# Optimization experiments

Hardware: AMD Instinct MI355X
Metric: run time of the kernel (lower is better)

Reference implementation:

```python
import jax, jax.numpy as jnp
import numpy as np

N_DST0 = 20000  # number of dst nodes of block0 == src nodes of block1


def _graph_conv(x, src, dst, n_dst, W, b):
    # DGL GraphConv with norm='both': D_in^{-1/2} A D_out^{-1/2} X W + b
    e_ones = jnp.ones(src.shape[0], dtype=x.dtype)
    deg_out = jax.ops.segment_sum(e_ones, src, num_segments=x.shape[0])
    deg_in = jax.ops.segment_sum(e_ones, dst, num_segments=n_dst)
    xs = x * jax.lax.rsqrt(jnp.maximum(deg_out, 1.0))[:, None]
    agg = jax.ops.segment_sum(xs[src], dst, num_segments=n_dst)  # [n_dst, F]
    agg = agg * jax.lax.rsqrt(jnp.maximum(deg_in, 1.0))[:, None]
    return agg @ W + b


def setup_inputs() -> dict:
    key = jax.random.key(0)
    ks = jax.random.split(key, 10)
    vocab, emb, hid, out = 50000, 128, 256, 16
    n_src0, n_dst0, n_dst1 = 50000, N_DST0, 5000
    e0, e1 = 300000, 75000
    return {
        "user_word": jax.random.randint(ks[0], (n_src0, 10, 5), 0, vocab),
        "labels": jax.random.randint(ks[1], (n_dst1,), 0, out),
        "src0": jax.random.randint(ks[2], (e0,), 0, n_src0),
        "dst0": jax.random.randint(ks[3], (e0,), 0, n_dst0),
        "src1": jax.random.randint(ks[4], (e1,), 0, n_dst0),
        "dst1": jax.random.randint(ks[5], (e1,), 0, n_dst1),
        "word_table": jax.random.normal(ks[6], (vocab, emb), jnp.float32),
        "W1": jax.random.normal(ks[7], (emb, hid), jnp.float32) * 0.05,
        "b1": jnp.zeros((hid,), jnp.float32),
        "W2": jax.random.normal(ks[8], (hid, out), jnp.float32) * 0.05,
        "b2": jnp.zeros((out,), jnp.float32),
    }


def reference(user_word, labels, src0, dst0, src1, dst1, word_table, W1, b1, W2, b2):
    n_dst1 = labels.shape[0]
    # embedding gather + mean over words (dim=2) then items (dim=1)
    wf = word_table[user_word]                    # [n_src0, n_items, n_words, emb]
    x = jnp.mean(jnp.mean(wf, axis=2), axis=1)    # [n_src0, emb]
    x = jax.nn.relu(_graph_conv(x, src0, dst0, N_DST0, W1, b1))
    x = jax.nn.relu(_graph_conv(x, src1, dst1, n_dst1, W2, b2))
    x = x[:n_dst1]
    return (x, labels)
```

## Files before the change

### kernel.cpp

```cpp
#include <hip/hip_runtime.h>

#define E0     300000
#define E1     75000
#define NSRC0  50000
#define NDST0  20000
#define NDST1  5000
#define EMB    128
#define HID    256
#define NOUT   16

#define NPB        40
#define TILE_SHIFT 12
#define NEMB_BLK   (NSRC0 / NPB)

#define X0S  32.0f
#define H1S  64.0f

typedef __attribute__((ext_vector_type(8))) short bf16x8;
typedef __attribute__((ext_vector_type(4))) float f32x4;
typedef __attribute__((ext_vector_type(2))) float f32x2;

__device__ __forceinline__ unsigned short f2bf(float f) {
    unsigned u = __float_as_uint(f);
    return (unsigned short)((u + 0x7FFFu + ((u >> 16) & 1u)) >> 16);
}
__device__ __forceinline__ unsigned pack2(float a, float b) {
    return (unsigned)f2bf(a) | ((unsigned)f2bf(b) << 16);
}
__device__ __forceinline__ unsigned pack4_fp8(float a0, float a1, float a2, float a3) {
    unsigned p = 0;
    p = __builtin_amdgcn_cvt_pk_fp8_f32(a0, a1, p, false);
    p = __builtin_amdgcn_cvt_pk_fp8_f32(a2, a3, p, true);
    return p;
}
__device__ __forceinline__ unsigned char f2fp8(float v) {
    unsigned p = __builtin_amdgcn_cvt_pk_fp8_f32(v, v, 0, false);
    return (unsigned char)(p & 0xFF);
}
#if __has_builtin(__builtin_amdgcn_cvt_pk_f32_fp8)
__device__ __forceinline__ f32x2 up_lo(unsigned v) { return __builtin_amdgcn_cvt_pk_f32_fp8(v, false); }
__device__ __forceinline__ f32x2 up_hi(unsigned v) { return __builtin_amdgcn_cvt_pk_f32_fp8(v, true); }
#else
__device__ __forceinline__ f32x2 up_lo(unsigned v) {
    f32x2 r; r.x = __builtin_amdgcn_cvt_f32_fp8(v, 0); r.y = __builtin_amdgcn_cvt_f32_fp8(v, 1); return r;
}
__device__ __forceinline__ f32x2 up_hi(unsigned v) {
    f32x2 r; r.x = __builtin_amdgcn_cvt_f32_fp8(v, 2); r.y = __builtin_amdgcn_cvt_f32_fp8(v, 3); return r;
}
#endif

__global__ void prep_kernel(const float* __restrict__ wt, unsigned char* __restrict__ wt8,
                            const float* __restrict__ W1, unsigned short* __restrict__ W1Tb,
                            const float* __restrict__ W2, unsigned short* __restrict__ W2Tb,
                            const int* __restrict__ src0, const int* __restrict__ dst0,
                            const int* __restrict__ src1, const int* __restrict__ dst1,
                            int* cnt0, int* cnt1, int* degO0, int* degO1) {
    int i = blockIdx.x * blockDim.x + threadIdx.x;
    if (i < NSRC0 * EMB / 8) {
        const float4* in = (const float4*)wt;
        float4 v0 = in[i * 2], v1 = in[i * 2 + 1];
        uint2 o;
        o.x = pack4_fp8(v0.x, v0.y, v0.z, v0.w);
        o.y = pack4_fp8(v1.x, v1.y, v1.z, v1.w);
        ((uint2*)wt8)[i] = o;
    }
    if (i < EMB * HID) {
        int n = i & 255, k = i >> 8;
        W1Tb[n * 128 + k] = f2bf(W1[i]);
    }
    if (i < HID * NOUT) {
        int n = i & 15, k = i >> 4;
        W2Tb[n * 256 + k] = f2bf(W2[i]);
    }
    if (i < E0) {
        atomicAdd(&cnt0[dst0[i]], 1);
        atomicAdd(&degO0[src0[i]], 1);
    }
    if (i < E1) {
        atomicAdd(&cnt1[dst1[i]], 1);
        atomicAdd(&degO1[src1[i]], 1);
    }
}

__device__ void scan_body(const int* __restrict__ cnt, int n,
                          int* __restrict__ off, int* __restrict__ cur) {
    __shared__ int sums[1024];
    int t = threadIdx.x;
    int chunk = (n + 1023) / 1024;
    int lo = t * chunk, hi = min(lo + chunk, n);
    int s = 0;
    for (int i = lo; i < hi; ++i) s += cnt[i];
    sums[t] = s;
    __syncthreads();
    for (int d = 1; d < 1024; d <<= 1) {
        int x = (t >= d) ? sums[t - d] : 0;
        __syncthreads();
        sums[t] += x;
        __syncthreads();
    }
    int run = (t == 0) ? 0 : sums[t - 1];
    for (int i = lo; i < hi; ++i) {
        off[i] = run; cur[i] = run;
        run += cnt[i];
    }
    if (t == 1023) off[n] = run;
}

__global__ void scan_kernel(const int* cnt0, int* off0, int* cur0,
                            const int* cnt1, int* off1, int* cur1) {
    if (blockIdx.x == 0) scan_body(cnt0, NDST0, off0, cur0);
    else                 scan_body(cnt1, NDST1, off1, cur1);
}

__global__ void embed_bucket_kernel(const int* __restrict__ user_word,
                                    const unsigned char* __restrict__ wt8,
                                    const int* __restrict__ degO0,
                                    unsigned char* __restrict__ x0f,
                                    const int* __restrict__ src0, const int* __restrict__ dst0,
                                    const int* __restrict__ src1, const int* __restrict__ dst1,
                                    int* cur0, int* cur1, int* esrc0, int* esrc1) {
    if (blockIdx.x & 1) {
        int i = (blockIdx.x >> 1) * 256 + threadIdx.x;
        if (i < E0) {
            int p = atomicAdd(&cur0[dst0[i]], 1);
            esrc0[p] = src0[i];
        }
        if (i < E1) {
            int p = atomicAdd(&cur1[dst1[i]], 1);
            esrc1[p] = src1[i];
        }
        return;
    }
    int eb = blockIdx.x >> 1;
    __shared__ int raw[NPB * 50];
    __shared__ int srt[NPB * 50];
    __shared__ int cnt[NPB * 17];
    int t = threadIdx.x;
    int base = eb * NPB * 50;
    for (int j = t; j < NPB * 50; j += 256)
        raw[j] = user_word[base + j];
    for (int j = t; j < NPB * 17; j += 256)
        cnt[j] = 0;
    __syncthreads();
    if (t < NPB) {
        int* c = cnt + t * 17;
        const int* r = raw + t * 50;
        for (int j = 0; j < 50; ++j) c[r[j] >> TILE_SHIFT]++;
        int run = 0;
        for (int b = 0; b < 13; ++b) { int v = c[b]; c[b] = run; run += v; }
        int* o = srt + t * 50;
        for (int j = 0; j < 50; ++j) { int v = r[j]; o[c[v >> TILE_SHIFT]++] = v; }
    }
    __syncthreads();
    int g = t >> 5, l = t & 31;
    const unsigned* wt4 = (const unsigned*)wt8;
    const int* id0 = srt + (g     ) * 50;
    const int* id1 = srt + (g +  8) * 50;
    const int* id2 = srt + (g + 16) * 50;
    const int* id3 = srt + (g + 24) * 50;
    const int* id4 = srt + (g + 32) * 50;
    f32x2 a01[5], a23[5];
    #pragma unroll
    for (int k = 0; k < 5; ++k) { a01[k] = (f32x2){0.f, 0.f}; a23[k] = (f32x2){0.f, 0.f}; }
    for (int j = 0; j < 50; j += 2) {
        unsigned v0a = wt4[id0[j] * 32 + l], v0b = wt4[id0[j + 1] * 32 + l];
        unsigned v1a = wt4[id1[j] * 32 + l], v1b = wt4[id1[j + 1] * 32 + l];
        unsigned v2a = wt4[id2[j] * 32 + l], v2b = wt4[id2[j + 1] * 32 + l];
        unsigned v3a = wt4[id3[j] * 32 + l], v3b = wt4[id3[j + 1] * 32 + l];
        unsigned v4a = wt4[id4[j] * 32 + l], v4b = wt4[id4[j + 1] * 32 + l];
        a01[0] += up_lo(v0a) + up_lo(v0b); a23[0] += up_hi(v0a) + up_hi(v0b);
        a01[1] += up_lo(v1a) + up_lo(v1b); a23[1] += up_hi(v1a) + up_hi(v1b);
        a01[2] += up_lo(v2a) + up_lo(v2b); a23[2] += up_hi(v2a) + up_hi(v2b);
        a01[3] += up_lo(v3a) + up_lo(v3b); a23[3] += up_hi(v3a) + up_hi(v3b);
        a01[4] += up_lo(v4a) + up_lo(v4b); a23[4] += up_hi(v4a) + up_hi(v4b);
    }
    #pragma unroll
    for (int k = 0; k < 5; ++k) {
        int node = eb * NPB + g + k * 8;
        float s = rsqrtf(fmaxf((float)degO0[node], 1.0f)) * (0.02f * X0S);
        ((unsigned*)x0f)[node * 32 + l] =
            pack4_fp8(a01[k].x * s, a01[k].y * s, a23[k].x * s, a23[k].y * s);
    }
}

__global__ void agg1_kernel(const int* __restrict__ off0, const int* __restrict__ esrc0,
                            const unsigned char* __restrict__ x0f,
                            unsigned short* __restrict__ agg1b) {
    int d = blockIdx.x;
    int t = threadIdx.x;
    int half = t >> 5, l = t & 31;
    int lo = off0[d], hi = off0[d + 1];
    const unsigned* x4 = (const unsigned*)x0f;
    f32x2 a01a = {0.f, 0.f}, a23a = {0.f, 0.f};
    f32x2 a01b = {0.f, 0.f}, a23b = {0.f, 0.f};
    int j = lo + half;
    for (; j + 2 < hi; j += 4) {
        unsigned va = x4[esrc0[j] * 32 + l];
        unsigned vb = x4[esrc0[j + 2] * 32 + l];
        a01a += up_lo(va); a23a += up_hi(va);
        a01b += up_lo(vb); a23b += up_hi(vb);
    }
    if (j < hi) {
        unsigned v = x4[esrc0[j] * 32 + l];
        a01a += up_lo(v); a23a += up_hi(v);
    }
    f32x2 a01 = a01a + a01b, a23 = a23a + a23b;
    a01.x += __shfl_down(a01.x, 32); a01.y += __shfl_down(a01.y, 32);
    a23.x += __shfl_down(a23.x, 32); a23.y += __shfl_down(a23.y, 32);
    if (half == 0) {
        float sc = rsqrtf(fmaxf((float)(hi - lo), 1.0f)) * (1.0f / X0S);
        uint2 o; o.x = pack2(a01.x * sc, a01.y * sc); o.y = pack2(a23.x * sc, a23.y * sc);
        ((uint2*)agg1b)[d * 32 + l] = o;
    }
}

__global__ void gemm1_kernel(const unsigned short* __restrict__ agg1b,
                             const int* __restrict__ degO1,
                             const unsigned short* __restrict__ W1Tb,
                             const float* __restrict__ b1,
                             unsigned char* __restrict__ h1f) {
    __shared__ float s_out[16];
    int t = threadIdx.x;
    int row0 = blockIdx.x * 16;
    if (t < 16) s_out[t] = rsqrtf(fmaxf((float)degO1[row0 + t], 1.0f)) * H1S;
    __syncthreads();
    int w = t >> 6, lane = t & 63;
    int m = lane & 15, quad = lane >> 4;
    const unsigned short* abase = agg1b + (row0 + m) * 128 + quad * 8;
    bf16x8 afr[4];
    #pragma unroll
    for (int ks = 0; ks < 4; ++ks)
        afr[ks] = *(const bf16x8*)(abase + ks * 32);
    #pragma unroll
    for (int ct = 0; ct < 4; ++ct) {
        int gcol0 = (w * 4 + ct) * 16;
        const unsigned short* bbase = W1Tb + (gcol0 + m) * 128 + quad * 8;
        f32x4 acc = {0.f, 0.f, 0.f, 0.f};
        #pragma unroll
        for (int ks = 0; ks < 4; ++ks) {
            bf16x8 bfr = *(const bf16x8*)(bbase + ks * 32);
            acc = __builtin_amdgcn_mfma_f32_16x16x32_bf16(afr[ks], bfr, acc, 0, 0, 0);
        }
        int gcol = gcol0 + m;
        float bb = b1[gcol];
        #pragma unroll
        for (int reg = 0; reg < 4; ++reg) {
            int row = quad * 4 + reg;
            h1f[(row0 + row) * 256 + gcol] = f2fp8(fmaxf(acc[reg] + bb, 0.f) * s_out[row]);
        }
    }
}

__global__ void agg2_kernel(const int* __restrict__ off1, const int* __restrict__ esrc1,
                            const unsigned char* __restrict__ h1f,
                            unsigned short* __restrict__ agg2b) {
    int d = blockIdx.x;
    int l = threadIdx.x;
    int lo = off1[d], hi = off1[d + 1];
    const unsigned* h4 = (const unsigned*)h1f;
    f32x2 a01 = {0.f, 0.f}, a23 = {0.f, 0.f};
    int j = lo;
    for (; j + 3 < hi; j += 4) {
        unsigned v0 = h4[esrc1[j] * 64 + l];
        unsigned v1 = h4[esrc1[j + 1] * 64 + l];
        unsigned v2 = h4[esrc1[j + 2] * 64 + l];
        unsigned v3 = h4[esrc1[j + 3] * 64 + l];
        a01 += up_lo(v0) + up_lo(v1) + up_lo(v2) + up_lo(v3);
        a23 += up_hi(v0) + up_hi(v1) + up_hi(v2) + up_hi(v3);
    }
    for (; j < hi; ++j) {
        unsigned v = h4[esrc1[j] * 64 + l];
        a01 += up_lo(v); a23 += up_hi(v);
    }
    float sc = rsqrtf(fmaxf((float)(hi - lo), 1.0f)) * (1.0f / H1S);
    uint2 o; o.x = pack2(a01.x * sc, a01.y * sc); o.y = pack2(a23.x * sc, a23.y * sc);
    ((uint2*)agg2b)[d * 64 + l] = o;
}

__global__ void gemm2_kernel(const unsigned short* __restrict__ agg2b,
                             const unsigned short* __restrict__ W2Tb,
                             const float* __restrict__ b2,
                             const int* __restrict__ labels,
                             float* __restrict__ out) {
    int lane = threadIdx.x;
    int row0 = blockIdx.x * 16;
    int m = lane & 15, quad = lane >> 4;
    int arow = min(row0 + m, NDST1 - 1);
    const unsigned short* abase = agg2b + arow * 256 + quad * 8;
    const unsigned short* bbase = W2Tb + m * 256 + quad * 8;
    f32x4 acc = {0.f, 0.f, 0.f, 0.f};
    #pragma unroll
    for (int ks = 0; ks < 8; ++ks) {
        bf16x8 af = *(const bf16x8*)(abase + ks * 32);
        bf16x8 bf = *(const bf16x8*)(bbase + ks * 32);
        acc = __builtin_amdgcn_mfma_f32_16x16x32_bf16(af, bf, acc, 0, 0, 0);
    }
    float bb = b2[m];
    #pragma unroll
    for (int reg = 0; reg < 4; ++reg) {
        int row = row0 + quad * 4 + reg;
        if (row < NDST1)
            out[row * NOUT + m] = fmaxf(acc[reg] + bb, 0.f);
    }
    if (lane < 16 && row0 + lane < NDST1)
        out[NDST1 * NOUT + row0 + lane] = (float)labels[row0 + lane];
}

extern "C" void kernel_launch(void* const* d_in, const int* in_sizes, int n_in,
                              void* d_out, int out_size, void* d_ws, size_t ws_size,
                              hipStream_t stream) {
    const int*   user_word  = (const int*)d_in[0];
    const int*   labels     = (const int*)d_in[1];
    const int*   src0       = (const int*)d_in[2];
    const int*   dst0       = (const int*)d_in[3];
    const int*   src1       = (const int*)d_in[4];
    const int*   dst1       = (const int*)d_in[5];
    const float* word_table = (const float*)d_in[6];
    const float* W1         = (const float*)d_in[7];
    const float* b1         = (const float*)d_in[8];
    const float* W2         = (const float*)d_in[9];
    const float* b2         = (const float*)d_in[10];

    int* iws = (int*)d_ws;
    int* cnt0  = iws;
    int* cnt1  = iws + 20000;
    int* degO0 = iws + 25000;
    int* degO1 = iws + 75000;
    int* off0  = iws + 95000;
    int* off1  = iws + 115001;
    int* cur0  = iws + 120002;
    int* cur1  = iws + 140002;
    int* esrc0 = iws + 145002;
    int* esrc1 = iws + 445002;
    unsigned char*  wt8   = (unsigned char*)(iws + 520004);
    unsigned char*  x0f   = (unsigned char*)(iws + 2120004);
    unsigned char*  h1f   = (unsigned char*)(iws + 3720004);
    unsigned short* agg1b = (unsigned short*)(iws + 5000004);
    unsigned short* agg2b = (unsigned short*)(iws + 6280004);
    unsigned short* W1Tb  = (unsigned short*)(iws + 6920004);
    unsigned short* W2Tb  = (unsigned short*)(iws + 6936388);

    hipMemsetAsync(iws, 0, 95000 * sizeof(int), stream);

    prep_kernel<<<(NSRC0 * EMB / 8 + 255) / 256, 256, 0, stream>>>(
        word_table, wt8, W1, W1Tb, W2, W2Tb,
        src0, dst0, src1, dst1, cnt0, cnt1, degO0, degO1);
    scan_kernel<<<2, 1024, 0, stream>>>(cnt0, off0, cur0, cnt1, off1, cur1);
    embed_bucket_kernel<<<NEMB_BLK * 2, 256, 0, stream>>>(
        user_word, wt8, degO0, x0f,
        src0, dst0, src1, dst1, cur0, cur1, esrc0, esrc1);
    agg1_kernel<<<NDST0, 64, 0, stream>>>(off0, esrc0, x0f, agg1b);
    gemm1_kernel<<<NDST0 / 16, 256, 0, stream>>>(agg1b, degO1, W1Tb, b1, h1f);
    agg2_kernel<<<NDST1, 64, 0, stream>>>(off1, esrc1, h1f, agg2b);
    gemm2_kernel<<<(NDST1 + 15) / 16, 64, 0, stream>>>(agg2b, W2Tb, b2, labels, (float*)d_out);
}
```

Baseline: 263.2 us.

## Fuse aggregation with GEMM per layer through shared-memory tiles

Merges agg1 and gemm1 into one layer1 kernel, and agg2 and gemm2 into one layer2 kernel. Each 1024-thread block aggregates 16 destination rows, one wave per row, into padded LDS tiles and then runs the MFMA GEMM straight from LDS. This removes two kernel launches and the global round trip of the bf16 aggregation buffers. In exchange, each wave in layer1 now computes one 16-column tile instead of four, and in layer2 only one wave of sixteen does the GEMM. Large blocks whose per-row edge counts vary may also lose occupancy or load balance.

```diff
diff --git a/kernel.cpp b/kernel.cpp
--- a/kernel.cpp
+++ b/kernel.cpp
@@ -183,127 +183,124 @@
     }
 }
 
-__global__ void agg1_kernel(const int* __restrict__ off0, const int* __restrict__ esrc0,
-                            const unsigned char* __restrict__ x0f,
-                            unsigned short* __restrict__ agg1b) {
-    int d = blockIdx.x;
-    int t = threadIdx.x;
-    int half = t >> 5, l = t & 31;
-    int lo = off0[d], hi = off0[d + 1];
-    const unsigned* x4 = (const unsigned*)x0f;
-    f32x2 a01a = {0.f, 0.f}, a23a = {0.f, 0.f};
-    f32x2 a01b = {0.f, 0.f}, a23b = {0.f, 0.f};
-    int j = lo + half;
-    for (; j + 2 < hi; j += 4) {
-        unsigned va = x4[esrc0[j] * 32 + l];
-        unsigned vb = x4[esrc0[j + 2] * 32 + l];
-        a01a += up_lo(va); a23a += up_hi(va);
-        a01b += up_lo(vb); a23b += up_hi(vb);
-    }
-    if (j < hi) {
-        unsigned v = x4[esrc0[j] * 32 + l];
-        a01a += up_lo(v); a23a += up_hi(v);
-    }
-    f32x2 a01 = a01a + a01b, a23 = a23a + a23b;
-    a01.x += __shfl_down(a01.x, 32); a01.y += __shfl_down(a01.y, 32);
-    a23.x += __shfl_down(a23.x, 32); a23.y += __shfl_down(a23.y, 32);
-    if (half == 0) {
-        float sc = rsqrtf(fmaxf((float)(hi - lo), 1.0f)) * (1.0f / X0S);
-        uint2 o; o.x = pack2(a01.x * sc, a01.y * sc); o.y = pack2(a23.x * sc, a23.y * sc);
-        ((uint2*)agg1b)[d * 32 + l] = o;
-    }
-}
-
-__global__ void gemm1_kernel(const unsigned short* __restrict__ agg1b,
-                             const int* __restrict__ degO1,
-                             const unsigned short* __restrict__ W1Tb,
-                             const float* __restrict__ b1,
-                             unsigned char* __restrict__ h1f) {
+__global__ void layer1_kernel(const int* __restrict__ off0, const int* __restrict__ esrc0,
+                              const unsigned char* __restrict__ x0f,
+                              const int* __restrict__ degO1,
+                              const unsigned short* __restrict__ W1Tb,
+                              const float* __restrict__ b1,
+                              unsigned char* __restrict__ h1f) {
+    __shared__ unsigned short A[16 * 136];
     __shared__ float s_out[16];
     int t = threadIdx.x;
     int row0 = blockIdx.x * 16;
+    int w = t >> 6, lane = t & 63;
+    int half = lane >> 5, l = lane & 31;
     if (t < 16) s_out[t] = rsqrtf(fmaxf((float)degO1[row0 + t], 1.0f)) * H1S;
-    __syncthreads();
+    {
+        int d = row0 + w;
+        int lo = off0[d], hi = off0[d + 1];
+        const unsigned* x4 = (const unsigned*)x0f;
+        f32x2 a01a = {0.f, 0.f}, a23a = {0.f, 0.f};
+        f32x2 a01b = {0.f, 0.f}, a23b = {0.f, 0.f};
+        int j = lo + half;
+        for (; j + 2 < hi; j += 4) {
+            unsigned va = x4[esrc0[j] * 32 + l];
+            unsigned vb = x4[esrc0[j + 2] * 32 + l];
+            a01a += up_lo(va); a23a += up_hi(va);
+            a01b += up_lo(vb); a23b += up_hi(vb);
+        }
+        if (j < hi) {
+            unsigned v = x4[esrc0[j] * 32 + l];
+            a01a += up_lo(v); a23a += up_hi(v);
+        }
+        f32x2 a01 = a01a + a01b, a23 = a23a + a23b;
+        a01.x += __shfl_down(a01.x, 32); a01.y += __shfl_down(a01.y, 32);
+        a23.x += __shfl_down(a23.x, 32); a23.y += __shfl_down(a23.y, 32);
+        if (half == 0) {
+            float sc = rsqrtf(fmaxf((float)(hi - lo), 1.0f)) * (1.0f / X0S);
+            uint2 o; o.x = pack2(a01.x * sc, a01.y * sc); o.y = pack2(a23.x * sc, a23.y * sc);
+            *(uint2*)(A + w * 136 + l * 4) = o;
+        }
+    }
+    __syncthreads();
+    int m = lane & 15, quad = lane >> 4;
+    bf16x8 afr[4];
+    #pragma unroll
+    for (int ks = 0; ks < 4; ++ks)
+        afr[ks] = *(const bf16x8*)(A + m * 136 + quad * 8 + ks * 32);
+    int gcol0 = w * 16;
+    const unsigned short* bbase = W1Tb + (gcol0 + m) * 128 + quad * 8;
+    f32x4 acc = {0.f, 0.f, 0.f, 0.f};
+    #pragma unroll
+    for (int ks = 0; ks < 4; ++ks) {
+        bf16x8 bfr = *(const bf16x8*)(bbase + ks * 32);
+        acc = __builtin_amdgcn_mfma_f32_16x16x32_bf16(afr[ks], bfr, acc, 0, 0, 0);
+    }
+    int gcol = gcol0 + m;
+    float bb = b1[gcol];
+    #pragma unroll
+    for (int reg = 0; reg < 4; ++reg) {
+        int row = quad * 4 + reg;
+        h1f[(row0 + row) * 256 + gcol] = f2fp8(fmaxf(acc[reg] + bb, 0.f) * s_out[row]);
+    }
+}
+
+__global__ void layer2_kernel(const int* __restrict__ off1, const int* __restrict__ esrc1,
+                              const unsigned char* __restrict__ h1f,
+                              const unsigned short* __restrict__ W2Tb,
+                              const float* __restrict__ b2,
+                              const int* __restrict__ labels,
+                              float* __restrict__ out) {
+    __shared__ unsigned short A[16 * 264];
+    int t = threadIdx.x;
+    int row0 = blockIdx.x * 16;
     int w = t >> 6, lane = t & 63;
-    int m = lane & 15, quad = lane >> 4;
-    const unsigned short* abase = agg1b + (row0 + m) * 128 + quad * 8;
-    bf16x8 afr[4];
-    #pragma unroll
-    for (int ks = 0; ks < 4; ++ks)
-        afr[ks] = *(const bf16x8*)(abase + ks * 32);
-    #pragma unroll
-    for (int ct = 0; ct < 4; ++ct) {
-        int gcol0 = (w * 4 + ct) * 16;
-        const unsigned short* bbase = W1Tb + (gcol0 + m) * 128 + quad * 8;
+    {
+        int d = row0 + w;
+        f32x2 a01 = {0.f, 0.f}, a23 = {0.f, 0.f};
+        float sc = 0.f;
+        if (d < NDST1) {
+            int lo = off1[d], hi = off1[d + 1];
+            const unsigned* h4 = (const unsigned*)h1f;
+            int j = lo;
+            for (; j + 3 < hi; j += 4) {
+                unsigned v0 = h4[esrc1[j] * 64 + lane];
+                unsigned v1 = h4[esrc1[j + 1] * 64 + lane];
+                unsigned v2 = h4[esrc1[j + 2] * 64 + lane];
+                unsigned v3 = h4[esrc1[j + 3] * 64 + lane];
+                a01 += up_lo(v0) + up_lo(v1) + up_lo(v2) + up_lo(v3);
+                a23 += up_hi(v0) + up_hi(v1) + up_hi(v2) + up_hi(v3);
+            }
+            for (; j < hi; ++j) {
+                unsigned v = h4[esrc1[j] * 64 + lane];
+                a01 += up_lo(v); a23 += up_hi(v);
+            }
+            sc = rsqrtf(fmaxf((float)(hi - lo), 1.0f)) * (1.0f / H1S);
+        }
+        uint2 o; o.x = pack2(a01.x * sc, a01.y * sc); o.y = pack2(a23.x * sc, a23.y * sc);
+        *(uint2*)(A + w * 264 + lane * 4) = o;
+    }
+    __syncthreads();
+    if (w == 0) {
+        int m = lane & 15, quad = lane >> 4;
+        const unsigned short* bbase = W2Tb + m * 256 + quad * 8;
         f32x4 acc = {0.f, 0.f, 0.f, 0.f};
         #pragma unroll
-        for (int ks = 0; ks < 4; ++ks) {
-            bf16x8 bfr = *(const bf16x8*)(bbase + ks * 32);
-            acc = __builtin_amdgcn_mfma_f32_16x16x32_bf16(afr[ks], bfr, acc, 0, 0, 0);
-        }
-        int gcol = gcol0 + m;
-        float bb = b1[gcol];
+        for (int ks = 0; ks < 8; ++ks) {
+            bf16x8 af = *(const bf16x8*)(A + m * 264 + quad * 8 + ks * 32);
+            bf16x8 bf = *(const bf16x8*)(bbase + ks * 32);
+            acc = __builtin_amdgcn_mfma_f32_16x16x32_bf16(af, bf, acc, 0, 0, 0);
+        }
+        float bb = b2[m];
         #pragma unroll
         for (int reg = 0; reg < 4; ++reg) {
-            int row = quad * 4 + reg;
-            h1f[(row0 + row) * 256 + gcol] = f2fp8(fmaxf(acc[reg] + bb, 0.f) * s_out[row]);
-        }
-    }
-}
-
-__global__ void agg2_kernel(const int* __restrict__ off1, const int* __restrict__ esrc1,
-                            const unsigned char* __restrict__ h1f,
-                            unsigned short* __restrict__ agg2b) {
-    int d = blockIdx.x;
-    int l = threadIdx.x;
-    int lo = off1[d], hi = off1[d + 1];
-    const unsigned* h4 = (const unsigned*)h1f;
-    f32x2 a01 = {0.f, 0.f}, a23 = {0.f, 0.f};
-    int j = lo;
-    for (; j + 3 < hi; j += 4) {
-        unsigned v0 = h4[esrc1[j] * 64 + l];
-        unsigned v1 = h4[esrc1[j + 1] * 64 + l];
-        unsigned v2 = h4[esrc1[j + 2] * 64 + l];
-        unsigned v3 = h4[esrc1[j + 3] * 64 + l];
-        a01 += up_lo(v0) + up_lo(v1) + up_lo(v2) + up_lo(v3);
-        a23 += up_hi(v0) + up_hi(v1) + up_hi(v2) + up_hi(v3);
-    }
-    for (; j < hi; ++j) {
-        unsigned v = h4[esrc1[j] * 64 + l];
-        a01 += up_lo(v); a23 += up_hi(v);
-    }
-    float sc = rsqrtf(fmaxf((float)(hi - lo), 1.0f)) * (1.0f / H1S);
-    uint2 o; o.x = pack2(a01.x * sc, a01.y * sc); o.y = pack2(a23.x * sc, a23.y * sc);
-    ((uint2*)agg2b)[d * 64 + l] = o;
-}
-
-__global__ void gemm2_kernel(const unsigned short* __restrict__ agg2b,
-                             const unsigned short* __restrict__ W2Tb,
-                             const float* __restrict__ b2,
-                             const int* __restrict__ labels,
-                             float* __restrict__ out) {
-    int lane = threadIdx.x;
-    int row0 = blockIdx.x * 16;
-    int m = lane & 15, quad = lane >> 4;
-    int arow = min(row0 + m, NDST1 - 1);
-    const unsigned short* abase = agg2b + arow * 256 + quad * 8;
-    const unsigned short* bbase = W2Tb + m * 256 + quad * 8;
-    f32x4 acc = {0.f, 0.f, 0.f, 0.f};
-    #pragma unroll
-    for (int ks = 0; ks < 8; ++ks) {
-        bf16x8 af = *(const bf16x8*)(abase + ks * 32);
-        bf16x8 bf = *(const bf16x8*)(bbase + ks * 32);
-        acc = __builtin_amdgcn_mfma_f32_16x16x32_bf16(af, bf, acc, 0, 0, 0);
-    }
-    float bb = b2[m];
-    #pragma unroll
-    for (int reg = 0; reg < 4; ++reg) {
-        int row = row0 + quad * 4 + reg;
-        if (row < NDST1)
-            out[row * NOUT + m] = fmaxf(acc[reg] + bb, 0.f);
-    }
-    if (lane < 16 && row0 + lane < NDST1)
-        out[NDST1 * NOUT + row0 + lane] = (float)labels[row0 + lane];
+            int row = row0 + quad * 4 + reg;
+            if (row < NDST1)
+                out[row * NOUT + m] = fmaxf(acc[reg] + bb, 0.f);
+        }
+        if (lane < 16 && row0 + lane < NDST1)
+            out[NDST1 * NOUT + row0 + lane] = (float)labels[row0 + lane];
+    }
 }
 
 extern "C" void kernel_launch(void* const* d_in, const int* in_sizes, int n_in,
@@ -332,13 +329,11 @@
     int* cur1  = iws + 140002;
     int* esrc0 = iws + 145002;
     int* esrc1 = iws + 445002;
-    unsigned char*  wt8   = (unsigned char*)(iws + 520004);
-    unsigned char*  x0f   = (unsigned char*)(iws + 2120004);
-    unsigned char*  h1f   = (unsigned char*)(iws + 3720004);
-    unsigned short* agg1b = (unsigned short*)(iws + 5000004);
-    unsigned short* agg2b = (unsigned short*)(iws + 6280004);
-    unsigned short* W1Tb  = (unsigned short*)(iws + 6920004);
-    unsigned short* W2Tb  = (unsigned short*)(iws + 6936388);
+    unsigned char*  wt8  = (unsigned char*)(iws + 520004);
+    unsigned char*  x0f  = (unsigned char*)(iws + 2120004);
+    unsigned char*  h1f  = (unsigned char*)(iws + 3720004);
+    unsigned short* W1Tb = (unsigned short*)(iws + 5000004);
+    unsigned short* W2Tb = (unsigned short*)(iws + 5008196);
 
     hipMemsetAsync(iws, 0, 95000 * sizeof(int), stream);
 
@@ -349,8 +344,7 @@
     embed_bucket_kernel<<<NEMB_BLK * 2, 256, 0, stream>>>(
         user_word, wt8, degO0, x0f,
         src0, dst0, src1, dst1, cur0, cur1, esrc0, esrc1);
-    agg1_kernel<<<NDST0, 64, 0, stream>>>(off0, esrc0, x0f, agg1b);
-    gemm1_kernel<<<NDST0 / 16, 256, 0, stream>>>(agg1b, degO1, W1Tb, b1, h1f);
-    agg2_kernel<<<NDST1, 64, 0, stream>>>(off1, esrc1, h1f, agg2b);
-    gemm2_kernel<<<(NDST1 + 15) / 16, 64, 0, stream>>>(agg2b, W2Tb, b2, labels, (float*)d_out);
-}
+    layer1_kernel<<<NDST0 / 16, 1024, 0, stream>>>(off0, esrc0, x0f, degO1, W1Tb, b1, h1f);
+    layer2_kernel<<<(NDST1 + 15) / 16, 1024, 0, stream>>>(off1, esrc1, h1f, W2Tb, b2,
+                                                          labels, (float*)d_out);
+}
```

Measured after the change: 258.6 us. About the same (-1.8%).
